# Kernel optimization log

Hardware: AMD Instinct MI355X
Metric: run time of the kernel (lower is better)

The kernel has to match this reference:

```python
import jax, jax.numpy as jnp
import numpy as np

D_MODEL = 1024
N_HEADS = 16
D_FF = 4096
EPS = 1e-5


def setup_inputs() -> dict:
    key = jax.random.key(0)
    ks = jax.random.split(key, 16)
    s = 0.02
    d, f = D_MODEL, D_FF
    return {
        "x": jax.random.normal(ks[0], (4, 2048, d), dtype=jnp.float32),
        "WQ": jax.random.normal(ks[1], (d, d), dtype=jnp.float32) * s,
        "bQ": jnp.zeros((d,), dtype=jnp.float32),
        "WK": jax.random.normal(ks[2], (d, d), dtype=jnp.float32) * s,
        "bK": jnp.zeros((d,), dtype=jnp.float32),
        "WV": jax.random.normal(ks[3], (d, d), dtype=jnp.float32) * s,
        "bV": jnp.zeros((d,), dtype=jnp.float32),
        "WO": jax.random.normal(ks[4], (d, d), dtype=jnp.float32) * s,
        "bO": jnp.zeros((d,), dtype=jnp.float32),
        "W1": jax.random.normal(ks[5], (f, d), dtype=jnp.float32) * s,
        "b1": jnp.zeros((f,), dtype=jnp.float32),
        "W2": jax.random.normal(ks[6], (d, f), dtype=jnp.float32) * s,
        "b2": jnp.zeros((d,), dtype=jnp.float32),
        "g1": jnp.ones((d,), dtype=jnp.float32),
        "be1": jnp.zeros((d,), dtype=jnp.float32),
        "g2": jnp.ones((d,), dtype=jnp.float32),
        "be2": jnp.zeros((d,), dtype=jnp.float32),
    }


def _layernorm(x, g, b):
    mu = jnp.mean(x, axis=-1, keepdims=True)
    var = jnp.mean(jnp.square(x - mu), axis=-1, keepdims=True)
    return (x - mu) * jax.lax.rsqrt(var + EPS) * g + b


def reference(x, WQ, bQ, WK, bK, WV, bV, WO, bO, W1, b1, W2, b2, g1, be1, g2, be2):
    B, T, D = x.shape
    H, dk = N_HEADS, D // N_HEADS
    # projections (torch Linear: x @ W.T + b), reshape to [B,H,T,dk]
    q = (x @ WQ.T + bQ).reshape(B, T, H, dk).transpose(0, 2, 1, 3)
    k = (x @ WK.T + bK).reshape(B, T, H, dk).transpose(0, 2, 1, 3)
    v = (x @ WV.T + bV).reshape(B, T, H, dk).transpose(0, 2, 1, 3)
    scores = jnp.einsum("bhqd,bhkd->bhqk", q, k) / jnp.sqrt(jnp.float32(dk))
    causal = jnp.tril(jnp.ones((T, T), dtype=bool))
    scores = jnp.where(causal[None, None], scores, jnp.float32(-jnp.inf))
    attn = jax.nn.softmax(scores, axis=-1)
    out = jnp.einsum("bhqk,bhkd->bhqd", attn, v)
    out = out.transpose(0, 2, 1, 3).reshape(B, T, D)
    attn_out = out @ WO.T + bO
    x = _layernorm(x + attn_out, g1, be1)
    ff = jax.nn.relu(x @ W1.T + b1) @ W2.T + b2
    return _layernorm(x + ff, g2, be2)
```

## Files before the change

kernel.cpp:

```cpp
#include <hip/hip_runtime.h>

typedef unsigned short u16;
typedef unsigned int u32;
typedef __bf16 bf16x8 __attribute__((ext_vector_type(8)));
typedef float f32x4 __attribute__((ext_vector_type(4)));

__device__ __forceinline__ u16 f2bf(float f) {
  u32 u = __builtin_bit_cast(u32, f);
  u = (u + 0x7fffu + ((u >> 16) & 1u)) >> 16;
  return (u16)u;
}
__device__ __forceinline__ float bf2f(u16 h) {
  return __builtin_bit_cast(float, ((u32)h) << 16);
}

__device__ __forceinline__ void gll16(const u16* g, u16* l) {
  __builtin_amdgcn_global_load_lds((const __attribute__((address_space(1))) void*)g,
                                   (__attribute__((address_space(3))) void*)l, 16, 0, 0);
}

__device__ __forceinline__ void barrier() {
  asm volatile("" ::: "memory");
  __builtin_amdgcn_s_barrier();
  asm volatile("" ::: "memory");
}
__device__ __forceinline__ void waitv8() { asm volatile("s_waitcnt vmcnt(8)" ::: "memory"); }
__device__ __forceinline__ void waitv0() { asm volatile("s_waitcnt vmcnt(0)" ::: "memory"); }
__device__ __forceinline__ void waitlgk0() { asm volatile("s_waitcnt lgkmcnt(0)" ::: "memory"); }

__global__ __launch_bounds__(256) void cvt_all(const float* __restrict__ x,
                                               const float* __restrict__ WQ,
                                               const float* __restrict__ WK,
                                               const float* __restrict__ WV,
                                               const float* __restrict__ WO,
                                               const float* __restrict__ W1,
                                               const float* __restrict__ W2,
                                               u16* __restrict__ xb,
                                               u16* __restrict__ wqkvb,
                                               u16* __restrict__ wob,
                                               u16* __restrict__ w1b,
                                               u16* __restrict__ w2b) {
  const int S = 1 << 20;
  int i = (blockIdx.x * 256 + threadIdx.x) * 4;
  const float* src;
  u16* dst;
  if (i < 8 * S) { src = x + i; dst = xb + i; }
  else {
    int j = i - 8 * S;
    if (j < 3 * S)      { src = (j < S) ? WQ + j : (j < 2 * S) ? WK + (j - S) : WV + (j - 2 * S);
                          dst = wqkvb + j; }
    else if (j < 4 * S) { src = WO + (j - 3 * S); dst = wob + (j - 3 * S); }
    else if (j < 8 * S) { src = W1 + (j - 4 * S); dst = w1b + (j - 4 * S); }
    else                { src = W2 + (j - 8 * S); dst = w2b + (j - 8 * S); }
  }
  float4 v = *(const float4*)src;
  uint2 o;
  o.x = (u32)f2bf(v.x) | ((u32)f2bf(v.y) << 16);
  o.y = (u32)f2bf(v.z) | ((u32)f2bf(v.w) << 16);
  *(uint2*)dst = o;
}

template <int RELU, int QKV, int SPLIT>
__global__ __launch_bounds__(512, 2) void gemm256(const u16* __restrict__ A,
                                                  const u16* __restrict__ W,
                                                  const float* __restrict__ bias0,
                                                  void* __restrict__ C0,
                                                  int M, int N, int K,
                                                  const float* __restrict__ bias1,
                                                  void* __restrict__ C1,
                                                  const float* __restrict__ bias2,
                                                  void* __restrict__ C2,
                                                  int NBN) {
  __shared__ alignas(16) u16 lds[4 * 16384];
  const int tid = threadIdx.x;
  const int id = blockIdx.x;
  const int xcd = id & 7, r = id >> 3;
  int bm, bn, kz = 0, koff = 0, KL = K;
  if (SPLIT) {
    bn = (r & 3) << 8;
    const int q = r >> 2;
    bm = ((q & 3) * 8 + xcd) << 8;
    kz = q >> 2;
    KL = K >> 1;
    koff = kz * KL;
  } else {
    bn = (r % NBN) << 8;
    bm = ((r / NBN) * 8 + xcd) << 8;
  }
  const int wave = tid >> 6, lane = tid & 63;
  const int lr = lane & 15, quad = lane >> 4;
  const int wm = (wave >> 2) << 7;
  const int wn = (wave & 3) << 6;

  const int lrow = lane >> 2;
  const int lch = (lane & 3) ^ ((lane >> 3) & 3);
  const u16* Asrc = A + (size_t)(bm + wave * 16 + lrow) * K + koff + lch * 8;
  const u16* Wsrc = W + (size_t)(bn + wave * 16 + lrow) * K + koff + lch * 8;
  const size_t half = (size_t)128 * K;
  u16* dstbase = lds + wave * 512;

  const int NT = KL >> 5;
  const int fro = (quad ^ ((lr >> 1) & 3)) * 8;
  f32x4 acc[8][4] = {};

  #pragma unroll
  for (int t = 0; t < 3; t++) {
    u16* d = dstbase + t * 16384;
    gll16(Asrc + (size_t)t * 32, d);
    gll16(Asrc + (size_t)t * 32 + half, d + 4096);
    gll16(Wsrc + (size_t)t * 32, d + 8192);
    gll16(Wsrc + (size_t)t * 32 + half, d + 12288);
  }
  waitv8();
  barrier();

  for (int t = 0; t < NT; t++) {
    const u16* sa = lds + (t & 3) * 16384;
    const u16* sb = sa + 8192;
    const int tp = (t + 3 < NT) ? t + 3 : NT - 1;
    u16* d = dstbase + ((t + 3) & 3) * 16384;
    const size_t ko = (size_t)tp * 32;

    bf16x8 af[4], bfr[4];
    #pragma unroll
    for (int mi = 0; mi < 4; mi++)
      af[mi] = *(const bf16x8*)(sa + (wm + mi * 16 + lr) * 32 + fro);
    #pragma unroll
    for (int ni = 0; ni < 4; ni++)
      bfr[ni] = *(const bf16x8*)(sb + (wn + ni * 16 + lr) * 32 + fro);
    gll16(Asrc + ko, d);
    gll16(Asrc + ko + half, d + 4096);
    barrier();
    waitlgk0();
    __builtin_amdgcn_s_setprio(1);
    #pragma unroll
    for (int mi = 0; mi < 4; mi++)
      #pragma unroll
      for (int ni = 0; ni < 4; ni++)
        acc[mi][ni] = __builtin_amdgcn_mfma_f32_16x16x32_bf16(af[mi], bfr[ni], acc[mi][ni], 0, 0, 0);
    __builtin_amdgcn_s_setprio(0);
    barrier();

    #pragma unroll
    for (int mi = 0; mi < 4; mi++)
      af[mi] = *(const bf16x8*)(sa + (wm + 64 + mi * 16 + lr) * 32 + fro);
    gll16(Wsrc + ko, d + 8192);
    gll16(Wsrc + ko + half, d + 12288);
    barrier();
    waitlgk0();
    __builtin_amdgcn_s_setprio(1);
    #pragma unroll
    for (int mi = 0; mi < 4; mi++)
      #pragma unroll
      for (int ni = 0; ni < 4; ni++)
        acc[4 + mi][ni] = __builtin_amdgcn_mfma_f32_16x16x32_bf16(af[mi], bfr[ni], acc[4 + mi][ni], 0, 0, 0);
    __builtin_amdgcn_s_setprio(0);
    waitv8();
    barrier();
  }
  waitv0();

  const float* bp = bias0;
  void* outp = C0;
  float scale = 1.0f;
  int cb = bn, Nout = N, seg = 0;
  if (QKV) {
    Nout = 1024;
    seg = bn >> 10;
    cb = bn & 1023;
    if (seg == 0) scale = 0.125f * 1.44269504089f;
    else if (seg == 1) { bp = bias1; outp = C1; }
    else { bp = bias2; outp = C2; }
  }
  if (SPLIT && kz) outp = C1;

  if (QKV && seg == 2) {
    #pragma unroll
    for (int ni = 0; ni < 4; ni++) {
      const int col = cb + wn + ni * 16 + lr;
      const int hh = col >> 6, dl = col & 63;
      const float bv = bp[col];
      #pragma unroll
      for (int mi = 0; mi < 8; mi++) {
        const int row0 = bm + wm + mi * 16 + quad * 4;
        const int bb = row0 >> 11, tt = row0 & 2047;
        u16 pk[4];
        #pragma unroll
        for (int rg = 0; rg < 4; rg++) pk[rg] = f2bf(acc[mi][ni][rg] + bv);
        uint2 val;
        val.x = (u32)pk[0] | ((u32)pk[1] << 16);
        val.y = (u32)pk[2] | ((u32)pk[3] << 16);
        *(uint2*)(((u16*)outp) + ((size_t)((bb * 16 + hh) * 64 + dl)) * 2048 + tt) = val;
      }
    }
    return;
  }

  #pragma unroll
  for (int ni = 0; ni < 4; ni++) {
    const int col = cb + wn + ni * 16 + lr;
    const float bv = (SPLIT && kz) ? 0.0f : bp[col];
    #pragma unroll
    for (int mi = 0; mi < 8; mi++) {
      #pragma unroll
      for (int rg = 0; rg < 4; rg++) {
        int row = bm + wm + mi * 16 + quad * 4 + rg;
        float v = (acc[mi][ni][rg] + bv) * scale;
        if (RELU) v = fmaxf(v, 0.0f);
        ((u16*)outp)[(size_t)row * Nout + col] = f2bf(v);
      }
    }
  }
}

constexpr int ALD = 72;

__global__ __launch_bounds__(256) void attn_mfma(const u16* __restrict__ qb,
                                                 const u16* __restrict__ kb,
                                                 const u16* __restrict__ vt,
                                                 u16* __restrict__ ctxb, int T) {
  __shared__ alignas(16) u16 sK[64 * 64];
  __shared__ alignas(16) u16 sVt[64 * 64];
  __shared__ alignas(16) u16 sP[4 * 2 * 16 * ALD];
  const int tid = threadIdx.x;
  const int i = blockIdx.x;
  const int g = (i & 7) | (((i >> 7) & 7) << 3);
  const int p = (i >> 3) & 15;
  const int h = g >> 2, b = g & 3;
  const size_t base = ((size_t)(b * T)) * 1024 + h * 64;
  const size_t vbase = ((size_t)((b * 16 + h) * 64)) * T;
  const int lane = tid & 63, wave = tid >> 6;
  const int lr = lane & 15, quad = lane >> 4;
  u16* sPA = sP + (wave * 2) * 16 * ALD;
  u16* sPB = sPA + 16 * ALD;

  const int srow = lane >> 3;
  const int sch = ((lane & 7) ^ srow) * 8;
  const int fsw = lr & 7;

  const int qtA = 31 - p, qtB = p;
  const int q0A = qtA * 64 + wave * 16, q0B = qtB * 64 + wave * 16;
  bf16x8 qfA[2], qfB[2];
  #pragma unroll
  for (int sl = 0; sl < 2; sl++) {
    uint4 uA = *(const uint4*)(qb + base + (size_t)(q0A + lr) * 1024 + sl * 32 + quad * 8);
    qfA[sl] = __builtin_bit_cast(bf16x8, uA);
    uint4 uB = *(const uint4*)(qb + base + (size_t)(q0B + lr) * 1024 + sl * 32 + quad * 8);
    qfB[sl] = __builtin_bit_cast(bf16x8, uB);
  }
  f32x4 oA[4] = {}, oB[4] = {};
  float smA[4] = {0, 0, 0, 0}, smB[4] = {0, 0, 0, 0};

  for (int kt = 0; kt <= qtA; kt++) {
    const bool doB = (kt <= qtB);
    __syncthreads();
    #pragma unroll
    for (int j = 0; j < 2; j++) {
      const int rowbase = (wave * 2 + j) * 8;
      const int r = rowbase + srow;
      gll16(kb + base + (size_t)(kt * 64 + r) * 1024 + sch, sK + rowbase * 64);
      gll16(vt + vbase + (size_t)r * T + (size_t)(kt * 64) + sch, sVt + rowbase * 64);
    }
    __syncthreads();

    f32x4 sa[4] = {}, sb[4] = {};
    #pragma unroll
    for (int sl = 0; sl < 2; sl++) {
      bf16x8 kf[4];
      #pragma unroll
      for (int nt = 0; nt < 4; nt++)
        kf[nt] = *(const bf16x8*)(sK + (nt * 16 + lr) * 64 + ((((sl << 2) | quad) ^ fsw) * 8));
      #pragma unroll
      for (int nt = 0; nt < 4; nt++)
        sa[nt] = __builtin_amdgcn_mfma_f32_16x16x32_bf16(kf[nt], qfA[sl], sa[nt], 0, 0, 0);
      if (doB) {
        #pragma unroll
        for (int nt = 0; nt < 4; nt++)
          sb[nt] = __builtin_amdgcn_mfma_f32_16x16x32_bf16(kf[nt], qfB[sl], sb[nt], 0, 0, 0);
      }
    }

    const int qloc = wave * 16 + lr;
    if (kt == qtA) {
      #pragma unroll
      for (int nt = 0; nt < 4; nt++)
        #pragma unroll
        for (int rg = 0; rg < 4; rg++)
          if (nt * 16 + quad * 4 + rg > qloc) sa[nt][rg] = -1e30f;
    }
    if (doB && kt == qtB) {
      #pragma unroll
      for (int nt = 0; nt < 4; nt++)
        #pragma unroll
        for (int rg = 0; rg < 4; rg++)
          if (nt * 16 + quad * 4 + rg > qloc) sb[nt][rg] = -1e30f;
    }

    #pragma unroll
    for (int nt = 0; nt < 4; nt++) {
      float e0 = __builtin_amdgcn_exp2f(sa[nt][0]);
      float e1 = __builtin_amdgcn_exp2f(sa[nt][1]);
      float e2 = __builtin_amdgcn_exp2f(sa[nt][2]);
      float e3 = __builtin_amdgcn_exp2f(sa[nt][3]);
      smA[nt] += (e0 + e1) + (e2 + e3);
      uint2 pk;
      pk.x = __builtin_amdgcn_perm(__builtin_bit_cast(u32, e1), __builtin_bit_cast(u32, e0), 0x07060302u);
      pk.y = __builtin_amdgcn_perm(__builtin_bit_cast(u32, e3), __builtin_bit_cast(u32, e2), 0x07060302u);
      *(uint2*)(sPA + lr * ALD + nt * 16 + quad * 4) = pk;
    }
    if (doB) {
      #pragma unroll
      for (int nt = 0; nt < 4; nt++) {
        float e0 = __builtin_amdgcn_exp2f(sb[nt][0]);
        float e1 = __builtin_amdgcn_exp2f(sb[nt][1]);
        float e2 = __builtin_amdgcn_exp2f(sb[nt][2]);
        float e3 = __builtin_amdgcn_exp2f(sb[nt][3]);
        smB[nt] += (e0 + e1) + (e2 + e3);
        uint2 pk;
        pk.x = __builtin_amdgcn_perm(__builtin_bit_cast(u32, e1), __builtin_bit_cast(u32, e0), 0x07060302u);
        pk.y = __builtin_amdgcn_perm(__builtin_bit_cast(u32, e3), __builtin_bit_cast(u32, e2), 0x07060302u);
        *(uint2*)(sPB + lr * ALD + nt * 16 + quad * 4) = pk;
      }
    }
    asm volatile("" ::: "memory");

    #pragma unroll
    for (int sl = 0; sl < 2; sl++) {
      bf16x8 vf[4];
      #pragma unroll
      for (int nt = 0; nt < 4; nt++)
        vf[nt] = *(const bf16x8*)(sVt + (nt * 16 + lr) * 64 + ((((sl << 2) | quad) ^ fsw) * 8));
      bf16x8 pfA = *(const bf16x8*)(sPA + lr * ALD + sl * 32 + quad * 8);
      #pragma unroll
      for (int nt = 0; nt < 4; nt++)
        oA[nt] = __builtin_amdgcn_mfma_f32_16x16x32_bf16(pfA, vf[nt], oA[nt], 0, 0, 0);
      if (doB) {
        bf16x8 pfB = *(const bf16x8*)(sPB + lr * ALD + sl * 32 + quad * 8);
        #pragma unroll
        for (int nt = 0; nt < 4; nt++)
          oB[nt] = __builtin_amdgcn_mfma_f32_16x16x32_bf16(pfB, vf[nt], oB[nt], 0, 0, 0);
      }
    }
  }

  float sumA = (smA[0] + smA[1]) + (smA[2] + smA[3]);
  sumA += __shfl_xor(sumA, 16);
  sumA += __shfl_xor(sumA, 32);
  float sumB = (smB[0] + smB[1]) + (smB[2] + smB[3]);
  sumB += __shfl_xor(sumB, 16);
  sumB += __shfl_xor(sumB, 32);
  float invA[4], invB[4];
  #pragma unroll
  for (int rg = 0; rg < 4; rg++) {
    invA[rg] = 1.0f / __shfl(sumA, quad * 4 + rg);
    invB[rg] = 1.0f / __shfl(sumB, quad * 4 + rg);
  }
  #pragma unroll
  for (int nt = 0; nt < 4; nt++)
    #pragma unroll
    for (int rg = 0; rg < 4; rg++) {
      int qrow = q0A + quad * 4 + rg;
      ctxb[base + (size_t)qrow * 1024 + nt * 16 + lr] = f2bf(oA[nt][rg] * invA[rg]);
    }
  #pragma unroll
  for (int nt = 0; nt < 4; nt++)
    #pragma unroll
    for (int rg = 0; rg < 4; rg++) {
      int qrow = q0B + quad * 4 + rg;
      ctxb[base + (size_t)qrow * 1024 + nt * 16 + lr] = f2bf(oB[nt][rg] * invB[rg]);
    }
}

template <int ABF>
__global__ __launch_bounds__(256) void ln_kernel(const void* __restrict__ a,
                                                 const u16* __restrict__ b,
                                                 const u16* __restrict__ c,
                                                 const float* __restrict__ g,
                                                 const float* __restrict__ be,
                                                 float* __restrict__ of32,
                                                 u16* __restrict__ obf) {
  const int row = blockIdx.x;
  const int tid = threadIdx.x;
  const size_t base = (size_t)row * 1024;
  const int cc = tid * 4;
  float a0, a1, a2, a3;
  if (ABF) {
    uint2 ua = *(const uint2*)((const u16*)a + base + cc);
    a0 = bf2f(ua.x & 0xffff); a1 = bf2f(ua.x >> 16);
    a2 = bf2f(ua.y & 0xffff); a3 = bf2f(ua.y >> 16);
  } else {
    float4 xa = *(const float4*)((const float*)a + base + cc);
    a0 = xa.x; a1 = xa.y; a2 = xa.z; a3 = xa.w;
  }
  uint2 ub = *(const uint2*)(b + base + cc);
  uint2 uc = *(const uint2*)(c + base + cc);
  float v0 = a0 + bf2f(ub.x & 0xffff) + bf2f(uc.x & 0xffff);
  float v1 = a1 + bf2f(ub.x >> 16)    + bf2f(uc.x >> 16);
  float v2 = a2 + bf2f(ub.y & 0xffff) + bf2f(uc.y & 0xffff);
  float v3 = a3 + bf2f(ub.y >> 16)    + bf2f(uc.y >> 16);
  float s1 = v0 + v1 + v2 + v3;
  float s2 = v0 * v0 + v1 * v1 + v2 * v2 + v3 * v3;
  for (int off = 1; off < 64; off <<= 1) {
    s1 += __shfl_xor(s1, off);
    s2 += __shfl_xor(s2, off);
  }
  __shared__ float red[8];
  int wv = tid >> 6;
  if ((tid & 63) == 0) { red[wv] = s1; red[4 + wv] = s2; }
  __syncthreads();
  s1 = red[0] + red[1] + red[2] + red[3];
  s2 = red[4] + red[5] + red[6] + red[7];
  float mu = s1 * (1.0f / 1024.0f);
  float var = s2 * (1.0f / 1024.0f) - mu * mu;
  float rs = rsqrtf(var + 1e-5f);
  float4 gv = *(const float4*)(g + cc);
  float4 bev = *(const float4*)(be + cc);
  float y0 = (v0 - mu) * rs * gv.x + bev.x;
  float y1 = (v1 - mu) * rs * gv.y + bev.y;
  float y2 = (v2 - mu) * rs * gv.z + bev.z;
  float y3 = (v3 - mu) * rs * gv.w + bev.w;
  if (of32) {
    float4 o = make_float4(y0, y1, y2, y3);
    *(float4*)(of32 + base + cc) = o;
  }
  if (obf) {
    uint2 o;
    o.x = (u32)f2bf(y0) | ((u32)f2bf(y1) << 16);
    o.y = (u32)f2bf(y2) | ((u32)f2bf(y3) << 16);
    *(uint2*)(obf + base + cc) = o;
  }
}

extern "C" void kernel_launch(void* const* d_in, const int* in_sizes, int n_in,
                              void* d_out, int out_size, void* d_ws, size_t ws_size,
                              hipStream_t stream) {
  const int Mtok = 8192, D = 1024, F = 4096, T = 2048;
  const float* x   = (const float*)d_in[0];
  const float* WQ  = (const float*)d_in[1];
  const float* bQ  = (const float*)d_in[2];
  const float* WK  = (const float*)d_in[3];
  const float* bK  = (const float*)d_in[4];
  const float* WV  = (const float*)d_in[5];
  const float* bV  = (const float*)d_in[6];
  const float* WO  = (const float*)d_in[7];
  const float* bO  = (const float*)d_in[8];
  const float* W1  = (const float*)d_in[9];
  const float* b1  = (const float*)d_in[10];
  const float* W2  = (const float*)d_in[11];
  const float* b2  = (const float*)d_in[12];
  const float* g1  = (const float*)d_in[13];
  const float* be1 = (const float*)d_in[14];
  const float* g2  = (const float*)d_in[15];
  const float* be2 = (const float*)d_in[16];

  char* ws = (char*)d_ws;
  const size_t MB = 1024 * 1024;
  u16*  xb     = (u16*)(ws + 0);
  u16*  wqkvb  = (u16*)(ws + 16 * MB);
  u16*  wob    = (u16*)(ws + 22 * MB);
  u16*  w1b    = (u16*)(ws + 24 * MB);
  u16*  w2b    = (u16*)(ws + 32 * MB);
  u16*  qb     = (u16*)(ws + 40 * MB);
  u16*  kb     = (u16*)(ws + 56 * MB);
  u16*  vtb    = (u16*)(ws + 72 * MB);
  u16*  ctxb   = (u16*)(ws + 88 * MB);
  u16*  wp0    = (u16*)(ws + 104 * MB);
  u16*  wp1    = (u16*)(ws + 120 * MB);
  u16*  h1b    = (u16*)(ws + 136 * MB);
  u16*  ff1b   = (u16*)(ws + 40 * MB);
  u16*  fp0    = (u16*)(ws + 0);
  u16*  fp1    = (u16*)(ws + 16 * MB);
  float* out   = (float*)d_out;

  dim3 blk(256);
  dim3 blk512(512);
  cvt_all<<<(20 << 20) / 1024, blk, 0, stream>>>(x, WQ, WK, WV, WO, W1, W2,
                                                 xb, wqkvb, wob, w1b, w2b);

  gemm256<0, 1, 0><<<dim3(384), blk512, 0, stream>>>(xb, wqkvb, bQ, qb, Mtok, 3072, D,
                                                     bK, kb, bV, vtb, 12);
  attn_mfma<<<dim3(1024), blk, 0, stream>>>(qb, kb, vtb, ctxb, T);

  gemm256<0, 0, 1><<<dim3(256), blk512, 0, stream>>>(ctxb, wob, bO, wp0, Mtok, D, D,
                                                     nullptr, wp1, nullptr, nullptr, 4);
  ln_kernel<0><<<Mtok, blk, 0, stream>>>(x, wp0, wp1, g1, be1, nullptr, h1b);

  gemm256<1, 0, 0><<<dim3(512), blk512, 0, stream>>>(h1b, w1b, b1, ff1b, Mtok, F, D,
                                                     nullptr, nullptr, nullptr, nullptr, 16);
  gemm256<0, 0, 1><<<dim3(256), blk512, 0, stream>>>(ff1b, w2b, b2, fp0, Mtok, D, F,
                                                     nullptr, fp1, nullptr, nullptr, 4);
  ln_kernel<1><<<Mtok, blk, 0, stream>>>(h1b, fp0, fp1, g2, be2, out, (u16*)nullptr);
}
```

Before: 505.1 us.

## Software-pipeline LDS fragment loads ahead of MFMA in GEMM main loop

Restructures the GEMM K-loop into a 2x unrolled ping-pong schedule. LDS fragment reads for the next half-tile are issued before the current MFMA block, with sched_barrier fences and no explicit lgkmcnt(0) wait, so LDS latency overlaps matrix math. It uses more fragment registers, which can lower occupancy, and it assumes NT is even. The changed barrier and prefetch ordering also risks LDS hazards.

```diff
diff --git a/kernel.cpp b/kernel.cpp
--- a/kernel.cpp
+++ b/kernel.cpp
@@ -26,7 +26,6 @@
 }
 __device__ __forceinline__ void waitv8() { asm volatile("s_waitcnt vmcnt(8)" ::: "memory"); }
 __device__ __forceinline__ void waitv0() { asm volatile("s_waitcnt vmcnt(0)" ::: "memory"); }
-__device__ __forceinline__ void waitlgk0() { asm volatile("s_waitcnt lgkmcnt(0)" ::: "memory"); }
 
 __global__ __launch_bounds__(256) void cvt_all(const float* __restrict__ x,
                                                const float* __restrict__ WQ,
@@ -103,6 +102,25 @@
   const int fro = (quad ^ ((lr >> 1) & 3)) * 8;
   f32x4 acc[8][4] = {};
 
+#define STAGE_A(tt) { const int tp_ = ((tt) < NT) ? (tt) : NT - 1;               \
+                      u16* d_ = dstbase + ((tt) & 3) * 16384;                    \
+                      const size_t ko_ = (size_t)tp_ * 32;                       \
+                      gll16(Asrc + ko_, d_); gll16(Asrc + ko_ + half, d_ + 4096); }
+#define STAGE_B(tt) { const int tp_ = ((tt) < NT) ? (tt) : NT - 1;               \
+                      u16* d_ = dstbase + ((tt) & 3) * 16384;                    \
+                      const size_t ko_ = (size_t)tp_ * 32;                       \
+                      gll16(Wsrc + ko_, d_ + 8192); gll16(Wsrc + ko_ + half, d_ + 12288); }
+#define LDA(dst, slot, roff) { const u16* s_ = lds + (slot) * 16384;             \
+    _Pragma("unroll") for (int mi_ = 0; mi_ < 4; mi_++)                          \
+      dst[mi_] = *(const bf16x8*)(s_ + (wm + (roff) + mi_ * 16 + lr) * 32 + fro); }
+#define LDB(dst, slot) { const u16* s_ = lds + (slot) * 16384 + 8192;            \
+    _Pragma("unroll") for (int ni_ = 0; ni_ < 4; ni_++)                          \
+      dst[ni_] = *(const bf16x8*)(s_ + (wn + ni_ * 16 + lr) * 32 + fro); }
+#define MFMA16(AF, BF, O)                                                        \
+    _Pragma("unroll") for (int mi_ = 0; mi_ < 4; mi_++)                          \
+    _Pragma("unroll") for (int ni_ = 0; ni_ < 4; ni_++)                          \
+      acc[(O) + mi_][ni_] = __builtin_amdgcn_mfma_f32_16x16x32_bf16(AF[mi_], BF[ni_], acc[(O) + mi_][ni_], 0, 0, 0);
+
   #pragma unroll
   for (int t = 0; t < 3; t++) {
     u16* d = dstbase + t * 16384;
@@ -114,51 +132,55 @@
   waitv8();
   barrier();
 
-  for (int t = 0; t < NT; t++) {
-    const u16* sa = lds + (t & 3) * 16384;
-    const u16* sb = sa + 8192;
-    const int tp = (t + 3 < NT) ? t + 3 : NT - 1;
-    u16* d = dstbase + ((t + 3) & 3) * 16384;
-    const size_t ko = (size_t)tp * 32;
-
-    bf16x8 af[4], bfr[4];
-    #pragma unroll
-    for (int mi = 0; mi < 4; mi++)
-      af[mi] = *(const bf16x8*)(sa + (wm + mi * 16 + lr) * 32 + fro);
-    #pragma unroll
-    for (int ni = 0; ni < 4; ni++)
-      bfr[ni] = *(const bf16x8*)(sb + (wn + ni * 16 + lr) * 32 + fro);
-    gll16(Asrc + ko, d);
-    gll16(Asrc + ko + half, d + 4096);
-    barrier();
-    waitlgk0();
+  bf16x8 aX[4], bX[4], aY[4], bY[4], a1f[4];
+  LDA(aX, 0, 0);
+  LDB(bX, 0);
+
+  for (int t = 0; t < NT; t += 2) {
+    STAGE_A(t + 3);
+    barrier();
+    LDA(a1f, t & 3, 64);
+    __builtin_amdgcn_sched_barrier(0);
     __builtin_amdgcn_s_setprio(1);
-    #pragma unroll
-    for (int mi = 0; mi < 4; mi++)
-      #pragma unroll
-      for (int ni = 0; ni < 4; ni++)
-        acc[mi][ni] = __builtin_amdgcn_mfma_f32_16x16x32_bf16(af[mi], bfr[ni], acc[mi][ni], 0, 0, 0);
+    MFMA16(aX, bX, 0);
     __builtin_amdgcn_s_setprio(0);
     barrier();
-
-    #pragma unroll
-    for (int mi = 0; mi < 4; mi++)
-      af[mi] = *(const bf16x8*)(sa + (wm + 64 + mi * 16 + lr) * 32 + fro);
-    gll16(Wsrc + ko, d + 8192);
-    gll16(Wsrc + ko + half, d + 12288);
-    barrier();
-    waitlgk0();
+    STAGE_B(t + 3);
+    waitv8();
+    barrier();
+    LDA(aY, (t + 1) & 3, 0);
+    LDB(bY, (t + 1) & 3);
+    __builtin_amdgcn_sched_barrier(0);
     __builtin_amdgcn_s_setprio(1);
-    #pragma unroll
-    for (int mi = 0; mi < 4; mi++)
-      #pragma unroll
-      for (int ni = 0; ni < 4; ni++)
-        acc[4 + mi][ni] = __builtin_amdgcn_mfma_f32_16x16x32_bf16(af[mi], bfr[ni], acc[4 + mi][ni], 0, 0, 0);
+    MFMA16(a1f, bX, 4);
     __builtin_amdgcn_s_setprio(0);
+    barrier();
+    STAGE_A(t + 4);
+    barrier();
+    LDA(a1f, (t + 1) & 3, 64);
+    __builtin_amdgcn_sched_barrier(0);
+    __builtin_amdgcn_s_setprio(1);
+    MFMA16(aY, bY, 0);
+    __builtin_amdgcn_s_setprio(0);
+    barrier();
+    STAGE_B(t + 4);
     waitv8();
     barrier();
+    LDA(aX, (t + 2) & 3, 0);
+    LDB(bX, (t + 2) & 3);
+    __builtin_amdgcn_sched_barrier(0);
+    __builtin_amdgcn_s_setprio(1);
+    MFMA16(a1f, bY, 4);
+    __builtin_amdgcn_s_setprio(0);
+    barrier();
   }
   waitv0();
+
+#undef STAGE_A
+#undef STAGE_B
+#undef LDA
+#undef LDB
+#undef MFMA16
 
   const float* bp = bias0;
   void* outp = C0;
```

Result: no change. 513.1 us (+1.6%).

## Double-buffer K/V tiles in attention kernel to overlap loads with compute

Applied to the files above, without the earlier changes.

Attention now keeps two LDS slots for K and V^T and issues the next tile's global-to-LDS loads before computing on the current tile, waiting only on the older loads with a partial vmcnt wait. This is meant to hide global load latency behind the MFMA and softmax work, in place of the load-then-sync pattern used before. It doubles the LDS used for K/V, which may lower occupancy, and issues one redundant clamped load on the final iteration. The GEMM change only inlines the lgkmcnt wait and has no effect.

```diff
diff --git a/kernel.cpp b/kernel.cpp
--- a/kernel.cpp
+++ b/kernel.cpp
@@ -25,8 +25,8 @@
   asm volatile("" ::: "memory");
 }
 __device__ __forceinline__ void waitv8() { asm volatile("s_waitcnt vmcnt(8)" ::: "memory"); }
+__device__ __forceinline__ void waitv4() { asm volatile("s_waitcnt vmcnt(4)" ::: "memory"); }
 __device__ __forceinline__ void waitv0() { asm volatile("s_waitcnt vmcnt(0)" ::: "memory"); }
-__device__ __forceinline__ void waitlgk0() { asm volatile("s_waitcnt lgkmcnt(0)" ::: "memory"); }
 
 __global__ __launch_bounds__(256) void cvt_all(const float* __restrict__ x,
                                                const float* __restrict__ WQ,
@@ -131,7 +131,7 @@
     gll16(Asrc + ko, d);
     gll16(Asrc + ko + half, d + 4096);
     barrier();
-    waitlgk0();
+    asm volatile("s_waitcnt lgkmcnt(0)" ::: "memory");
     __builtin_amdgcn_s_setprio(1);
     #pragma unroll
     for (int mi = 0; mi < 4; mi++)
@@ -147,7 +147,7 @@
     gll16(Wsrc + ko, d + 8192);
     gll16(Wsrc + ko + half, d + 12288);
     barrier();
-    waitlgk0();
+    asm volatile("s_waitcnt lgkmcnt(0)" ::: "memory");
     __builtin_amdgcn_s_setprio(1);
     #pragma unroll
     for (int mi = 0; mi < 4; mi++)
@@ -219,8 +219,8 @@
                                                  const u16* __restrict__ kb,
                                                  const u16* __restrict__ vt,
                                                  u16* __restrict__ ctxb, int T) {
-  __shared__ alignas(16) u16 sK[64 * 64];
-  __shared__ alignas(16) u16 sVt[64 * 64];
+  __shared__ alignas(16) u16 sK[2][64 * 64];
+  __shared__ alignas(16) u16 sVt[2][64 * 64];
   __shared__ alignas(16) u16 sP[4 * 2 * 16 * ALD];
   const int tid = threadIdx.x;
   const int i = blockIdx.x;
@@ -239,6 +239,16 @@
   const int fsw = lr & 7;
 
   const int qtA = 31 - p, qtB = p;
+
+#define STAGEKV(ktt, slot) {                                                       \
+    const int kc_ = ((ktt) <= qtA) ? (ktt) : qtA;                                  \
+    _Pragma("unroll") for (int j_ = 0; j_ < 2; j_++) {                             \
+      const int rb_ = (wave * 2 + j_) * 8;                                         \
+      const int rr_ = rb_ + srow;                                                  \
+      gll16(kb + base + (size_t)(kc_ * 64 + rr_) * 1024 + sch, sK[slot] + rb_ * 64);\
+      gll16(vt + vbase + (size_t)rr_ * T + (size_t)(kc_ * 64) + sch, sVt[slot] + rb_ * 64);\
+    } }
+
   const int q0A = qtA * 64 + wave * 16, q0B = qtB * 64 + wave * 16;
   bf16x8 qfA[2], qfB[2];
   #pragma unroll
@@ -251,17 +261,16 @@
   f32x4 oA[4] = {}, oB[4] = {};
   float smA[4] = {0, 0, 0, 0}, smB[4] = {0, 0, 0, 0};
 
+  STAGEKV(0, 0);
+
   for (int kt = 0; kt <= qtA; kt++) {
     const bool doB = (kt <= qtB);
-    __syncthreads();
-    #pragma unroll
-    for (int j = 0; j < 2; j++) {
-      const int rowbase = (wave * 2 + j) * 8;
-      const int r = rowbase + srow;
-      gll16(kb + base + (size_t)(kt * 64 + r) * 1024 + sch, sK + rowbase * 64);
-      gll16(vt + vbase + (size_t)r * T + (size_t)(kt * 64) + sch, sVt + rowbase * 64);
-    }
-    __syncthreads();
+    barrier();
+    STAGEKV(kt + 1, (kt + 1) & 1);
+    waitv4();
+    barrier();
+    const u16* sKc = sK[kt & 1];
+    const u16* sVc = sVt[kt & 1];
 
     f32x4 sa[4] = {}, sb[4] = {};
     #pragma unroll
@@ -269,7 +278,7 @@
       bf16x8 kf[4];
       #pragma unroll
       for (int nt = 0; nt < 4; nt++)
-        kf[nt] = *(const bf16x8*)(sK + (nt * 16 + lr) * 64 + ((((sl << 2) | quad) ^ fsw) * 8));
+        kf[nt] = *(const bf16x8*)(sKc + (nt * 16 + lr) * 64 + ((((sl << 2) | quad) ^ fsw) * 8));
       #pragma unroll
       for (int nt = 0; nt < 4; nt++)
         sa[nt] = __builtin_amdgcn_mfma_f32_16x16x32_bf16(kf[nt], qfA[sl], sa[nt], 0, 0, 0);
@@ -329,7 +338,7 @@
       bf16x8 vf[4];
       #pragma unroll
       for (int nt = 0; nt < 4; nt++)
-        vf[nt] = *(const bf16x8*)(sVt + (nt * 16 + lr) * 64 + ((((sl << 2) | quad) ^ fsw) * 8));
+        vf[nt] = *(const bf16x8*)(sVc + (nt * 16 + lr) * 64 + ((((sl << 2) | quad) ^ fsw) * 8));
       bf16x8 pfA = *(const bf16x8*)(sPA + lr * ALD + sl * 32 + quad * 8);
       #pragma unroll
       for (int nt = 0; nt < 4; nt++)
@@ -342,6 +351,8 @@
       }
     }
   }
+  waitv0();
+#undef STAGEKV
 
   float sumA = (smA[0] + smA[1]) + (smA[2] + smA[3]);
   sumA += __shfl_xor(sumA, 16);
```

New measurement: 504.7 us. No clear change (-0.1%).
